# Kernel tuning notes

Measured on AMD Instinct MI355X. Metric: run time of the kernel, lower is better.

The kernel has to match this reference:

```python
import jax, jax.numpy as jnp
import numpy as np

NUM_NODES = 100000
NFEAT = 128
EMBED_DIM = 128
NHEADS = 2
NHID = EMBED_DIM // NHEADS  # 64
REL_DIM = 128
NUM_REL = 500
E1 = 288000  # 1-hop edges
E2 = 32000   # 2-hop edges
E = E1 + E2
ALPHA = 0.2  # LeakyReLU slope
EPS = 1e-16


def setup_inputs() -> dict:
    key = jax.random.key(0)
    ks = jax.random.split(key, 10)
    edge_index = jax.random.randint(ks[0], (2, E), 0, NUM_NODES, dtype=jnp.int32)
    x = jax.random.normal(ks[1], (NUM_NODES, NFEAT), dtype=jnp.float32)
    r = jax.random.normal(ks[2], (NUM_REL, REL_DIM), dtype=jnp.float32)
    edge_type = jax.random.randint(ks[3], (E1,), 0, NUM_REL, dtype=jnp.int32)
    edge_type_nhop = jax.random.randint(ks[4], (E2, 2), 0, NUM_REL, dtype=jnp.int32)
    # learned params (get_param -> xavier-ish normal)
    s = 0.02
    W_heads = jax.random.normal(ks[5], (NHEADS, 2 * NFEAT + REL_DIM, NHID), dtype=jnp.float32) * s
    a_heads = jax.random.normal(ks[6], (NHEADS, NHID, 1), dtype=jnp.float32) * s
    W_out = jax.random.normal(ks[7], (2 * (NHID * NHEADS) + EMBED_DIM, NHEADS * NHID), dtype=jnp.float32) * s
    a_out = jax.random.normal(ks[8], (NHEADS * NHID, 1), dtype=jnp.float32) * s
    W_r = jax.random.normal(ks[9], (REL_DIM, EMBED_DIM), dtype=jnp.float32) * s
    return {"edge_index": edge_index, "x": x, "r": r, "edge_type": edge_type,
            "edge_type_nhop": edge_type_nhop, "W_heads": W_heads, "a_heads": a_heads,
            "W_out": W_out, "a_out": a_out, "W_r": W_r}


def _gat_layer(edge_index, x, edge_embed, W, a, concat):
    src = edge_index[0]
    dst = edge_index[1]
    # [E, 2*in + rel] -> [E, out]
    edge_h = jnp.concatenate([x[src], x[dst], edge_embed], axis=1) @ W
    e = jax.nn.leaky_relu(jnp.squeeze(edge_h @ a, axis=-1), negative_slope=ALPHA)  # [E]
    # segment softmax over src groups
    seg_max = jax.ops.segment_max(e, src, num_segments=NUM_NODES)
    w = jnp.exp(e - seg_max[src])
    denom = jax.ops.segment_sum(w, src, num_segments=NUM_NODES)
    att = w / (denom[src] + EPS)  # dropout p=0.0 -> identity
    out = jax.ops.segment_sum(att[:, None] * edge_h, src, num_segments=NUM_NODES)  # [N, out]
    return jax.nn.elu(out) if concat else out


def reference(edge_index, x, r, edge_type, edge_type_nhop, W_heads, a_heads, W_out, a_out, W_r):
    # first-pass relation edge embeddings
    edge_embed = jnp.concatenate(
        [r[edge_type], r[edge_type_nhop[:, 0]] + r[edge_type_nhop[:, 1]]], axis=0)  # [E, rel]
    # multi-head attention layers (concat heads)
    heads = [_gat_layer(edge_index, x, edge_embed, W_heads[h], a_heads[h], True)
             for h in range(NHEADS)]
    x1 = jnp.concatenate(heads, axis=1)  # [N, nheads*nhid]; dropout p=0 identity
    # transform relations
    r2 = r @ W_r  # [num_rel, embed_dim]
    edge_embed2 = jnp.concatenate(
        [r2[edge_type], r2[edge_type_nhop[:, 0]] + r2[edge_type_nhop[:, 1]]], axis=0)
    out = jax.nn.elu(_gat_layer(edge_index, x1, edge_embed2, W_out, a_out, False))
    return out, r2
```

## Files before the change

### kernel.cpp

```cpp
#include <hip/hip_runtime.h>
#include <math.h>

#define NNODES 100000
#define NREL 500
#define E1 288000
#define ETOT 320000
#define LALPHA 0.2f
#define SEPS 1e-16f
#define NB_SCAN ((NNODES + 255) / 256)
#define GTILES 6250
#define GTPB 5
#define GGRID (GTILES / GTPB)

typedef __attribute__((ext_vector_type(8))) short bf16x8;
typedef __attribute__((ext_vector_type(4))) float f32x4;

__device__ __forceinline__ unsigned short f2bf(float x) {
  unsigned int u = __float_as_uint(x);
  unsigned int r = (u + 0x7fffu + ((u >> 16) & 1u)) >> 16;
  return (unsigned short)r;
}
__device__ __forceinline__ unsigned int packbf2(float lo, float hi) {
  return (unsigned int)f2bf(lo) | ((unsigned int)f2bf(hi) << 16);
}
__device__ __forceinline__ float unpk_lo(unsigned int u) { return __uint_as_float(u << 16); }
__device__ __forceinline__ float unpk_hi(unsigned int u) {
  return __uint_as_float(u & 0xffff0000u);
}
__device__ __forceinline__ float lrelu(float e) { return (e >= 0.f) ? e : LALPHA * e; }
__device__ __forceinline__ float wexp(float lg) { return __expf(fminf(lg, 60.f)); }

__device__ __forceinline__ float wave_sum64(float v) {
#pragma unroll
  for (int o = 32; o >= 1; o >>= 1) v += __shfl_xor(v, o, 64);
  return v;
}
__device__ __forceinline__ float red16(float v) {
  v += __shfl_xor(v, 1, 64);
  v += __shfl_xor(v, 2, 64);
  v += __shfl_xor(v, 4, 64);
  v += __shfl_xor(v, 8, 64);
  return v;
}

__global__ void k_zero_int(int* __restrict__ p, int n) {
  int i = blockIdx.x * blockDim.x + threadIdx.x;
  if (i < n) p[i] = 0;
}

__global__ void k_count(const int* __restrict__ src, int* __restrict__ cnt) {
  int e = blockIdx.x * blockDim.x + threadIdx.x;
  if (e < ETOT) atomicAdd(&cnt[src[e]], 1);
}

__global__ void k_scan_a(const int* __restrict__ cnt, int* __restrict__ rowstart,
                         int* __restrict__ blockTot) {
  __shared__ int s[256];
  int t = threadIdx.x;
  int idx = blockIdx.x * 256 + t;
  int v = (idx < NNODES) ? cnt[idx] : 0;
  s[t] = v;
  __syncthreads();
  for (int off = 1; off < 256; off <<= 1) {
    int xv = (t >= off) ? s[t - off] : 0;
    __syncthreads();
    s[t] += xv;
    __syncthreads();
  }
  if (idx < NNODES) rowstart[idx] = s[t] - v;
  if (t == 255) blockTot[blockIdx.x] = s[255];
}

__global__ void k_scan_b(const int* __restrict__ blockTot, int* __restrict__ blockOff) {
  __shared__ int s[512];
  int t = threadIdx.x;
  int v = (t < NB_SCAN) ? blockTot[t] : 0;
  s[t] = v;
  __syncthreads();
  for (int off = 1; off < 512; off <<= 1) {
    int xv = (t >= off) ? s[t - off] : 0;
    __syncthreads();
    s[t] += xv;
    __syncthreads();
  }
  if (t < NB_SCAN) blockOff[t] = s[t] - v;
}

__global__ void k_scan_c(int* __restrict__ rowstart, const int* __restrict__ blockOff,
                         int* __restrict__ cursor) {
  int idx = blockIdx.x * 256 + threadIdx.x;
  if (idx < NNODES) {
    int v = rowstart[idx] + blockOff[blockIdx.x];
    rowstart[idx] = v;
    cursor[idx] = v;
  }
  if (idx == 0) rowstart[NNODES] = ETOT;
}

__global__ void k_scatter(const int* __restrict__ src, int* __restrict__ cursor,
                          int* __restrict__ perm) {
  int e = blockIdx.x * blockDim.x + threadIdx.x;
  if (e < ETOT) {
    int pos = atomicAdd(&cursor[src[e]], 1);
    perm[pos] = e;
  }
}

__global__ void k_relprep1(const float* __restrict__ r, const float* __restrict__ Wh,
                           const float* __restrict__ ah, unsigned int* __restrict__ rW1p,
                           float* __restrict__ srel1) {
  __shared__ float vals[128];
  int t = blockIdx.x;
  int tid = threadIdx.x;
  int h = tid >> 6, kk = tid & 63;
  const float* wcol = Wh + h * 24576 + 256 * 64 + kk;
  const float* rrow = r + t * 128;
  float acc = 0.f;
#pragma unroll 4
  for (int d = 0; d < 128; ++d) acc = fmaf(rrow[d], wcol[d * 64], acc);
  vals[tid] = acc;
  float p = wave_sum64(acc * ah[h * 64 + kk]);
  if (kk == 0) srel1[t * 2 + h] = p;
  __syncthreads();
  if (tid < 64) rW1p[t * 64 + tid] = packbf2(vals[2 * tid], vals[2 * tid + 1]);
}

__global__ void k_relprep2f(const float* __restrict__ r, const float* __restrict__ Wr,
                            const float* __restrict__ Wo, const float* __restrict__ ao,
                            unsigned int* __restrict__ rW2p, float* __restrict__ srel2,
                            float* __restrict__ r2out) {
  __shared__ float v2[128];
  __shared__ float s[128];
  __shared__ float vals[128];
  int t = blockIdx.x;
  int k = threadIdx.x;
  float a2 = 0.f;
#pragma unroll 4
  for (int d = 0; d < 128; ++d) a2 = fmaf(r[t * 128 + d], Wr[d * 128 + k], a2);
  r2out[t * 128 + k] = a2;
  v2[k] = a2;
  __syncthreads();
  float acc = 0.f;
#pragma unroll 4
  for (int d = 0; d < 128; ++d) acc = fmaf(v2[d], Wo[(256 + d) * 128 + k], acc);
  vals[k] = acc;
  s[k] = acc * ao[k];
  __syncthreads();
  for (int off = 64; off >= 1; off >>= 1) {
    if (k < off) s[k] += s[k + off];
    __syncthreads();
  }
  if (k == 0) srel2[t] = s[0];
  if (k < 64) rW2p[t * 64 + k] = packbf2(vals[2 * k], vals[2 * k + 1]);
}

__global__ void k_packb_both(const float* __restrict__ Wh, const float* __restrict__ Wo,
                             unsigned short* __restrict__ Wb1,
                             unsigned short* __restrict__ Wb2) {
  int c = blockIdx.x & 255;
  int layer = blockIdx.x >> 8;
  int d = threadIdx.x;
  if (layer == 0) {
    int h = (c >> 6) & 1, part = c >> 7, kc = c & 63;
    Wb1[c * 128 + d] = f2bf(Wh[h * 24576 + (part * 128 + d) * 64 + kc]);
  } else {
    int part = c >> 7, kc = c & 127;
    Wb2[c * 128 + d] = f2bf(Wo[(part * 128 + d) * 128 + kc]);
  }
}

template <int LAYER>
__global__ __launch_bounds__(256) void k_gemm_mfma(const void* __restrict__ Xin,
                                                   const unsigned short* __restrict__ Wb,
                                                   const float* __restrict__ avec,
                                                   unsigned int* __restrict__ xWp,
                                                   float* __restrict__ sc) {
  const int lane = threadIdx.x & 63;
  const int wave = threadIdx.x >> 6;
  const int colv = lane & 15;
  const int kg = lane >> 4;

  bf16x8 b[4][4];
#pragma unroll
  for (int t = 0; t < 4; ++t)
#pragma unroll
    for (int s = 0; s < 4; ++s)
      b[t][s] = *(const bf16x8*)(Wb + (size_t)(wave * 64 + t * 16 + colv) * 128 + s * 32 +
                                 kg * 8);
  float av[4];
#pragma unroll
  for (int t = 0; t < 4; ++t) av[t] = avec[(wave & 1) * 64 + t * 16 + colv];
  const int slot = (LAYER == 1) ? (((wave & 1) << 1) | (wave >> 1)) : wave;

  const float4* xf4 = (const float4*)Xin;
  const uint4* xu4 = (const uint4*)Xin;
  int tile = blockIdx.x * GTPB;

  float4 cf[8];
  uint4 cu[4];
  {
    int ar = tile * 16 + colv;
    if (LAYER == 1) {
      int base = ar * 32 + kg * 2;
#pragma unroll
      for (int s = 0; s < 4; ++s) {
        cf[2 * s] = xf4[base + s * 8];
        cf[2 * s + 1] = xf4[base + s * 8 + 1];
      }
    } else {
      int base = ar * 16 + kg;
#pragma unroll
      for (int s = 0; s < 4; ++s) cu[s] = xu4[base + s * 4];
    }
  }

  for (int it = 0; it < GTPB; ++it, ++tile) {
    float4 nf[8];
    uint4 nu[4];
    const bool hasnext = (it + 1 < GTPB);
    if (hasnext) {
      int ar = (tile + 1) * 16 + colv;
      if (LAYER == 1) {
        int base = ar * 32 + kg * 2;
#pragma unroll
        for (int s = 0; s < 4; ++s) {
          nf[2 * s] = xf4[base + s * 8];
          nf[2 * s + 1] = xf4[base + s * 8 + 1];
        }
      } else {
        int base = ar * 16 + kg;
#pragma unroll
        for (int s = 0; s < 4; ++s) nu[s] = xu4[base + s * 4];
      }
    }

    bf16x8 a[4];
    if (LAYER == 1) {
#pragma unroll
      for (int s = 0; s < 4; ++s) {
        union {
          unsigned short us[8];
          bf16x8 v;
        } u;
        u.us[0] = f2bf(cf[2 * s].x); u.us[1] = f2bf(cf[2 * s].y);
        u.us[2] = f2bf(cf[2 * s].z); u.us[3] = f2bf(cf[2 * s].w);
        u.us[4] = f2bf(cf[2 * s + 1].x); u.us[5] = f2bf(cf[2 * s + 1].y);
        u.us[6] = f2bf(cf[2 * s + 1].z); u.us[7] = f2bf(cf[2 * s + 1].w);
        a[s] = u.v;
      }
    } else {
#pragma unroll
      for (int s = 0; s < 4; ++s) {
        union {
          uint4 q;
          bf16x8 v;
        } u;
        u.q = cu[s];
        a[s] = u.v;
      }
    }

    f32x4 acc[4];
#pragma unroll
    for (int t = 0; t < 4; ++t) acc[t] = (f32x4){0.f, 0.f, 0.f, 0.f};
#pragma unroll
    for (int s = 0; s < 4; ++s)
#pragma unroll
      for (int t = 0; t < 4; ++t)
        acc[t] = __builtin_amdgcn_mfma_f32_16x16x32_bf16(a[s], b[t][s], acc[t], 0, 0, 0);

    const int rbase = tile * 16 + kg * 4;
    const int m = colv >> 1;
    const bool evn = (colv & 1) == 0;
#pragma unroll
    for (int i = 0; i < 4; ++i) {
      unsigned int* orow = xWp + (size_t)(rbase + i) * 128 + wave * 32;
#pragma unroll
      for (int t = 0; t < 4; ++t) {
        float lo = acc[t][i];
        float other = __shfl_xor(lo, 1, 64);
        if (evn) orow[t * 8 + m] = packbf2(lo, other);
      }
      float p = 0.f;
#pragma unroll
      for (int t = 0; t < 4; ++t) p = fmaf(acc[t][i], av[t], p);
      p = red16(p);
      if (colv == 0) sc[(size_t)(rbase + i) * 4 + slot] = p;
    }

    if (hasnext) {
      if (LAYER == 1) {
#pragma unroll
        for (int j = 0; j < 8; ++j) cf[j] = nf[j];
      } else {
#pragma unroll
        for (int j = 0; j < 4; ++j) cu[j] = nu[j];
      }
    }
  }
}

__global__ void k_eprep1(const int* __restrict__ perm, const int* __restrict__ srcA,
                         const int* __restrict__ dstA, const int* __restrict__ et,
                         const int* __restrict__ et2, const float* __restrict__ sc1,
                         const float* __restrict__ srel1, int* __restrict__ srcp,
                         int* __restrict__ dnp, int2* __restrict__ t12,
                         float2* __restrict__ wexp1, float* __restrict__ denom1) {
  int p = blockIdx.x * 256 + threadIdx.x;
  if (p >= ETOT) return;
  int ed = perm[p];
  int src = srcA[ed], dn = dstA[ed];
  int t1, t2 = -1;
  float rel0, rel1;
  if (ed < E1) {
    t1 = et[ed];
    float2 sr = ((const float2*)srel1)[t1];
    rel0 = sr.x;
    rel1 = sr.y;
  } else {
    int2 tt = ((const int2*)et2)[ed - E1];
    t1 = tt.x;
    t2 = tt.y;
    float2 sa = ((const float2*)srel1)[t1];
    float2 sb = ((const float2*)srel1)[t2];
    rel0 = sa.x + sb.x;
    rel1 = sa.y + sb.y;
  }
  float4 ssv = ((const float4*)sc1)[src];
  float4 sdv = ((const float4*)sc1)[dn];
  float w0 = wexp(lrelu(ssv.x + sdv.y + rel0));
  float w1 = wexp(lrelu(ssv.z + sdv.w + rel1));
  wexp1[p] = make_float2(w0, w1);
  atomicAdd(&denom1[2 * src], w0);
  atomicAdd(&denom1[2 * src + 1], w1);
  srcp[p] = src;
  dnp[p] = dn;
  t12[p] = make_int2(t1, t2);
}

__global__ void k_eprep2(const int* __restrict__ srcp, const int* __restrict__ dnp,
                         const int2* __restrict__ t12, const float* __restrict__ sc2,
                         const float* __restrict__ srel2, float* __restrict__ wexp2,
                         float* __restrict__ denom2) {
  int p = blockIdx.x * 256 + threadIdx.x;
  if (p >= ETOT) return;
  int src = srcp[p], dn = dnp[p];
  int2 tt = t12[p];
  float rel = srel2[tt.x];
  if (tt.y >= 0) rel += srel2[tt.y];
  float4 ssv = ((const float4*)sc2)[src];
  float4 sdv = ((const float4*)sc2)[dn];
  float w = wexp(lrelu((ssv.x + ssv.y) + (sdv.z + sdv.w) + rel));
  wexp2[p] = w;
  atomicAdd(&denom2[src], w);
}

__global__ __launch_bounds__(256) void k_agg1(
    const int* __restrict__ rowstart, const float2* __restrict__ wexp1,
    const int* __restrict__ dnp, const int2* __restrict__ t12,
    const unsigned int* __restrict__ xWp, const unsigned int* __restrict__ rW1p,
    const float2* __restrict__ denom1, unsigned int* __restrict__ x1b) {
  int n = blockIdx.x * 4 + (threadIdx.x >> 6);
  int lane = threadIdx.x & 63;
  int q = lane & 15, g = lane >> 4;
  int s0 = rowstart[n];
  int deg = rowstart[n + 1] - s0;
  int jj = q + 16 * g;
  float r0 = 0.f, r1 = 0.f;
  if (deg > 0) {
    float ac0[4] = {0.f, 0.f, 0.f, 0.f}, ac1[4] = {0.f, 0.f, 0.f, 0.f};
    const int pend = s0 + deg;
    for (int p0 = s0; p0 < pend; p0 += 4) {
      int p = p0 + g;
      float w0 = 0.f, w1 = 0.f;
      int dne = 0, t1e = 0, t2e = -1;
      if (p < pend) {
        float2 wv = wexp1[p];
        w0 = wv.x;
        w1 = wv.y;
        dne = dnp[p];
        int2 tt = t12[p];
        t1e = tt.x;
        t2e = tt.y;
      }
      const unsigned int* xr = xWp + (size_t)dne * 128 + 64;
      const unsigned int* rp = rW1p + (size_t)t1e * 64;
#pragma unroll
      for (int k = 0; k < 4; ++k) {
        int j2 = q + 16 * k;
        float as = (k < 2) ? w0 : w1;
        unsigned int ud = xr[j2];
        unsigned int ur = rp[j2];
        float rv0 = unpk_lo(ur), rv1 = unpk_hi(ur);
        if (t2e >= 0) {
          unsigned int u2 = rW1p[(size_t)t2e * 64 + j2];
          rv0 += unpk_lo(u2);
          rv1 += unpk_hi(u2);
        }
        ac0[k] = fmaf(as, unpk_lo(ud) + rv0, ac0[k]);
        ac1[k] = fmaf(as, unpk_hi(ud) + rv1, ac1[k]);
      }
    }
#pragma unroll
    for (int k = 0; k < 4; ++k) {
      ac0[k] += __shfl_xor(ac0[k], 16, 64);
      ac0[k] += __shfl_xor(ac0[k], 32, 64);
      ac1[k] += __shfl_xor(ac1[k], 16, 64);
      ac1[k] += __shfl_xor(ac1[k], 32, 64);
    }
    float a0g = (g == 0) ? ac0[0] : (g == 1) ? ac0[1] : (g == 2) ? ac0[2] : ac0[3];
    float a1g = (g == 0) ? ac1[0] : (g == 1) ? ac1[1] : (g == 2) ? ac1[2] : ac1[3];
    float2 dd = denom1[n];
    float dsel = (g < 2) ? dd.x : dd.y;
    float isel = 1.f / (dsel + SEPS);
    unsigned int us = xWp[(size_t)n * 128 + jj];
    float o0 = (a0g + dsel * unpk_lo(us)) * isel;
    float o1 = (a1g + dsel * unpk_hi(us)) * isel;
    r0 = (o0 > 0.f) ? o0 : __expf(o0) - 1.f;
    r1 = (o1 > 0.f) ? o1 : __expf(o1) - 1.f;
  }
  x1b[(size_t)n * 64 + jj] = packbf2(r0, r1);
}

__global__ __launch_bounds__(256) void k_agg2(
    const int* __restrict__ rowstart, const float* __restrict__ wexp2,
    const int* __restrict__ dnp, const int2* __restrict__ t12,
    const unsigned int* __restrict__ xWp, const unsigned int* __restrict__ rW2p,
    const float* __restrict__ denom2, float* __restrict__ outp) {
  int n = blockIdx.x * 4 + (threadIdx.x >> 6);
  int lane = threadIdx.x & 63;
  int q = lane & 15, g = lane >> 4;
  int s0 = rowstart[n];
  int deg = rowstart[n + 1] - s0;
  int jj = q + 16 * g;
  float r0 = 0.f, r1 = 0.f;
  if (deg > 0) {
    float ac0[4] = {0.f, 0.f, 0.f, 0.f}, ac1[4] = {0.f, 0.f, 0.f, 0.f};
    const int pend = s0 + deg;
    for (int p0 = s0; p0 < pend; p0 += 4) {
      int p = p0 + g;
      float w = 0.f;
      int dne = 0, t1e = 0, t2e = -1;
      if (p < pend) {
        w = wexp2[p];
        dne = dnp[p];
        int2 tt = t12[p];
        t1e = tt.x;
        t2e = tt.y;
      }
      const unsigned int* xr = xWp + (size_t)dne * 128 + 64;
      const unsigned int* rp = rW2p + (size_t)t1e * 64;
#pragma unroll
      for (int k = 0; k < 4; ++k) {
        int j2 = q + 16 * k;
        unsigned int ud = xr[j2];
        unsigned int ur = rp[j2];
        float rv0 = unpk_lo(ur), rv1 = unpk_hi(ur);
        if (t2e >= 0) {
          unsigned int u2 = rW2p[(size_t)t2e * 64 + j2];
          rv0 += unpk_lo(u2);
          rv1 += unpk_hi(u2);
        }
        ac0[k] = fmaf(w, unpk_lo(ud) + rv0, ac0[k]);
        ac1[k] = fmaf(w, unpk_hi(ud) + rv1, ac1[k]);
      }
    }
#pragma unroll
    for (int k = 0; k < 4; ++k) {
      ac0[k] += __shfl_xor(ac0[k], 16, 64);
      ac0[k] += __shfl_xor(ac0[k], 32, 64);
      ac1[k] += __shfl_xor(ac1[k], 16, 64);
      ac1[k] += __shfl_xor(ac1[k], 32, 64);
    }
    float a0g = (g == 0) ? ac0[0] : (g == 1) ? ac0[1] : (g == 2) ? ac0[2] : ac0[3];
    float a1g = (g == 0) ? ac1[0] : (g == 1) ? ac1[1] : (g == 2) ? ac1[2] : ac1[3];
    float d = denom2[n];
    float inv = 1.f / (d + SEPS);
    unsigned int us = xWp[(size_t)n * 128 + jj];
    float o0 = (a0g + d * unpk_lo(us)) * inv;
    float o1 = (a1g + d * unpk_hi(us)) * inv;
    r0 = (o0 > 0.f) ? o0 : __expf(o0) - 1.f;
    r1 = (o1 > 0.f) ? o1 : __expf(o1) - 1.f;
  }
  ((float2*)outp)[(size_t)n * 64 + jj] = make_float2(r0, r1);
}

extern "C" void kernel_launch(void* const* d_in, const int* in_sizes, int n_in, void* d_out,
                              int out_size, void* d_ws, size_t ws_size, hipStream_t stream) {
  const int* edge_index = (const int*)d_in[0];
  const int* srcA = edge_index;
  const int* dstA = edge_index + ETOT;
  const float* x = (const float*)d_in[1];
  const float* r = (const float*)d_in[2];
  const int* et = (const int*)d_in[3];
  const int* et2 = (const int*)d_in[4];
  const float* Wh = (const float*)d_in[5];
  const float* ah = (const float*)d_in[6];
  const float* Wo = (const float*)d_in[7];
  const float* ao = (const float*)d_in[8];
  const float* Wr = (const float*)d_in[9];
  float* out = (float*)d_out;
  float* r2out = out + (size_t)NNODES * 128;

  char* ws = (char*)d_ws;
  size_t o = 0;
  auto alloc = [&](size_t bytes) {
    char* p = ws + o;
    o += (bytes + 255) & ~(size_t)255;
    return p;
  };
  unsigned int* xWp = (unsigned int*)alloc((size_t)NNODES * 128 * 4);
  float* sc1 = (float*)alloc((size_t)NNODES * 4 * 4);
  float* sc2 = (float*)alloc((size_t)NNODES * 4 * 4);
  int* zb = (int*)alloc((size_t)4 * NNODES * 4);
  int* cnt = zb;
  float* denom1 = (float*)(zb + NNODES);
  float* denom2 = (float*)(zb + 3 * NNODES);
  unsigned int* rW1p = (unsigned int*)alloc((size_t)NREL * 64 * 4);
  float* srel1 = (float*)alloc(2 * NREL * 4);
  unsigned int* rW2p = (unsigned int*)alloc((size_t)NREL * 64 * 4);
  float* srel2 = (float*)alloc(NREL * 4);
  unsigned int* x1b = (unsigned int*)alloc((size_t)NNODES * 64 * 4);
  unsigned short* Wb1 = (unsigned short*)alloc(256 * 128 * 2);
  unsigned short* Wb2 = (unsigned short*)alloc(256 * 128 * 2);
  int* rowstart = (int*)alloc((NNODES + 1) * 4);
  int* cursor = (int*)alloc(NNODES * 4);
  int* blockTot = (int*)alloc(512 * 4);
  int* blockOff = (int*)alloc(512 * 4);
  int* perm = (int*)alloc(ETOT * 4);
  int* srcp = (int*)alloc(ETOT * 4);
  int* dnp = (int*)alloc(ETOT * 4);
  int2* t12 = (int2*)alloc((size_t)ETOT * 8);
  float2* wexp1 = (float2*)alloc((size_t)ETOT * 8);
  float* wexp2 = (float*)alloc(ETOT * 4);

  const int EB = (ETOT + 255) / 256;

  k_zero_int<<<(4 * NNODES + 255) / 256, 256, 0, stream>>>(zb, 4 * NNODES);

  k_count<<<EB, 256, 0, stream>>>(srcA, cnt);
  k_scan_a<<<NB_SCAN, 256, 0, stream>>>(cnt, rowstart, blockTot);
  k_scan_b<<<1, 512, 0, stream>>>(blockTot, blockOff);
  k_scan_c<<<NB_SCAN, 256, 0, stream>>>(rowstart, blockOff, cursor);
  k_scatter<<<EB, 256, 0, stream>>>(srcA, cursor, perm);

  k_relprep1<<<NREL, 128, 0, stream>>>(r, Wh, ah, rW1p, srel1);
  k_relprep2f<<<NREL, 128, 0, stream>>>(r, Wr, Wo, ao, rW2p, srel2, r2out);
  k_packb_both<<<512, 128, 0, stream>>>(Wh, Wo, Wb1, Wb2);

  k_gemm_mfma<1><<<GGRID, 256, 0, stream>>>(x, Wb1, ah, xWp, sc1);
  k_eprep1<<<EB, 256, 0, stream>>>(perm, srcA, dstA, et, et2, sc1, srel1, srcp, dnp, t12,
                                   wexp1, denom1);
  k_agg1<<<NNODES / 4, 256, 0, stream>>>(rowstart, wexp1, dnp, t12, xWp, rW1p,
                                         (const float2*)denom1, x1b);

  k_gemm_mfma<2><<<GGRID, 256, 0, stream>>>(x1b, Wb2, ao, xWp, sc2);
  k_eprep2<<<EB, 256, 0, stream>>>(srcp, dnp, t12, sc2, srel2, wexp2, denom2);
  k_agg2<<<NNODES / 4, 256, 0, stream>>>(rowstart, wexp2, dnp, t12, xWp, rW2p, denom2, out);
}
```

Baseline: 428.0 us.

## Fuse edge-score and softmax-denominator computation into CSR aggregation kernels

The scatter kernel now writes destination and relation types directly in CSR order, which removes the permutation array and the separate per-edge prep pass. Both aggregation kernels compute the attention logits and exp weights inline, summing the softmax denominator per node with wave shuffles instead of global atomics. This drops two kernel launches, the wexp/denom/srcp buffers and their atomic traffic. In exchange the aggregation inner loop does extra gathers of destination scores and relation scalars per edge.

```diff
diff --git a/kernel.cpp b/kernel.cpp
--- a/kernel.cpp
+++ b/kernel.cpp
@@ -97,12 +97,23 @@
   if (idx == 0) rowstart[NNODES] = ETOT;
 }
 
-__global__ void k_scatter(const int* __restrict__ src, int* __restrict__ cursor,
-                          int* __restrict__ perm) {
+__global__ void k_scatter(const int* __restrict__ srcA, const int* __restrict__ dstA,
+                          const int* __restrict__ et, const int* __restrict__ et2,
+                          int* __restrict__ cursor, int* __restrict__ dnp,
+                          int2* __restrict__ t12) {
   int e = blockIdx.x * blockDim.x + threadIdx.x;
   if (e < ETOT) {
-    int pos = atomicAdd(&cursor[src[e]], 1);
-    perm[pos] = e;
+    int pos = atomicAdd(&cursor[srcA[e]], 1);
+    dnp[pos] = dstA[e];
+    int t1, t2 = -1;
+    if (e < E1) {
+      t1 = et[e];
+    } else {
+      int2 tt = ((const int2*)et2)[e - E1];
+      t1 = tt.x;
+      t2 = tt.y;
+    }
+    t12[pos] = make_int2(t1, t2);
   }
 }
 
@@ -300,66 +311,11 @@
   }
 }
 
-__global__ void k_eprep1(const int* __restrict__ perm, const int* __restrict__ srcA,
-                         const int* __restrict__ dstA, const int* __restrict__ et,
-                         const int* __restrict__ et2, const float* __restrict__ sc1,
-                         const float* __restrict__ srel1, int* __restrict__ srcp,
-                         int* __restrict__ dnp, int2* __restrict__ t12,
-                         float2* __restrict__ wexp1, float* __restrict__ denom1) {
-  int p = blockIdx.x * 256 + threadIdx.x;
-  if (p >= ETOT) return;
-  int ed = perm[p];
-  int src = srcA[ed], dn = dstA[ed];
-  int t1, t2 = -1;
-  float rel0, rel1;
-  if (ed < E1) {
-    t1 = et[ed];
-    float2 sr = ((const float2*)srel1)[t1];
-    rel0 = sr.x;
-    rel1 = sr.y;
-  } else {
-    int2 tt = ((const int2*)et2)[ed - E1];
-    t1 = tt.x;
-    t2 = tt.y;
-    float2 sa = ((const float2*)srel1)[t1];
-    float2 sb = ((const float2*)srel1)[t2];
-    rel0 = sa.x + sb.x;
-    rel1 = sa.y + sb.y;
-  }
-  float4 ssv = ((const float4*)sc1)[src];
-  float4 sdv = ((const float4*)sc1)[dn];
-  float w0 = wexp(lrelu(ssv.x + sdv.y + rel0));
-  float w1 = wexp(lrelu(ssv.z + sdv.w + rel1));
-  wexp1[p] = make_float2(w0, w1);
-  atomicAdd(&denom1[2 * src], w0);
-  atomicAdd(&denom1[2 * src + 1], w1);
-  srcp[p] = src;
-  dnp[p] = dn;
-  t12[p] = make_int2(t1, t2);
-}
-
-__global__ void k_eprep2(const int* __restrict__ srcp, const int* __restrict__ dnp,
-                         const int2* __restrict__ t12, const float* __restrict__ sc2,
-                         const float* __restrict__ srel2, float* __restrict__ wexp2,
-                         float* __restrict__ denom2) {
-  int p = blockIdx.x * 256 + threadIdx.x;
-  if (p >= ETOT) return;
-  int src = srcp[p], dn = dnp[p];
-  int2 tt = t12[p];
-  float rel = srel2[tt.x];
-  if (tt.y >= 0) rel += srel2[tt.y];
-  float4 ssv = ((const float4*)sc2)[src];
-  float4 sdv = ((const float4*)sc2)[dn];
-  float w = wexp(lrelu((ssv.x + ssv.y) + (sdv.z + sdv.w) + rel));
-  wexp2[p] = w;
-  atomicAdd(&denom2[src], w);
-}
-
 __global__ __launch_bounds__(256) void k_agg1(
-    const int* __restrict__ rowstart, const float2* __restrict__ wexp1,
-    const int* __restrict__ dnp, const int2* __restrict__ t12,
-    const unsigned int* __restrict__ xWp, const unsigned int* __restrict__ rW1p,
-    const float2* __restrict__ denom1, unsigned int* __restrict__ x1b) {
+    const int* __restrict__ rowstart, const int* __restrict__ dnp,
+    const int2* __restrict__ t12, const unsigned int* __restrict__ xWp,
+    const unsigned int* __restrict__ rW1p, const float* __restrict__ sc1,
+    const float2* __restrict__ srel1, unsigned int* __restrict__ x1b) {
   int n = blockIdx.x * 4 + (threadIdx.x >> 6);
   int lane = threadIdx.x & 63;
   int q = lane & 15, g = lane >> 4;
@@ -368,20 +324,32 @@
   int jj = q + 16 * g;
   float r0 = 0.f, r1 = 0.f;
   if (deg > 0) {
+    float4 scn = ((const float4*)sc1)[n];
+    const float ss0 = scn.x, ss1 = scn.z;
     float ac0[4] = {0.f, 0.f, 0.f, 0.f}, ac1[4] = {0.f, 0.f, 0.f, 0.f};
+    float dsum0 = 0.f, dsum1 = 0.f;
     const int pend = s0 + deg;
     for (int p0 = s0; p0 < pend; p0 += 4) {
       int p = p0 + g;
       float w0 = 0.f, w1 = 0.f;
       int dne = 0, t1e = 0, t2e = -1;
       if (p < pend) {
-        float2 wv = wexp1[p];
-        w0 = wv.x;
-        w1 = wv.y;
         dne = dnp[p];
         int2 tt = t12[p];
         t1e = tt.x;
         t2e = tt.y;
+        float2 sr = srel1[t1e];
+        float rel0 = sr.x, rel1 = sr.y;
+        if (t2e >= 0) {
+          float2 sb = srel1[t2e];
+          rel0 += sb.x;
+          rel1 += sb.y;
+        }
+        float4 sdv = ((const float4*)sc1)[dne];
+        w0 = wexp(lrelu(ss0 + sdv.y + rel0));
+        w1 = wexp(lrelu(ss1 + sdv.w + rel1));
+        dsum0 += w0;
+        dsum1 += w1;
       }
       const unsigned int* xr = xWp + (size_t)dne * 128 + 64;
       const unsigned int* rp = rW1p + (size_t)t1e * 64;
@@ -408,10 +376,13 @@
       ac1[k] += __shfl_xor(ac1[k], 16, 64);
       ac1[k] += __shfl_xor(ac1[k], 32, 64);
     }
+    dsum0 += __shfl_xor(dsum0, 16, 64);
+    dsum0 += __shfl_xor(dsum0, 32, 64);
+    dsum1 += __shfl_xor(dsum1, 16, 64);
+    dsum1 += __shfl_xor(dsum1, 32, 64);
     float a0g = (g == 0) ? ac0[0] : (g == 1) ? ac0[1] : (g == 2) ? ac0[2] : ac0[3];
     float a1g = (g == 0) ? ac1[0] : (g == 1) ? ac1[1] : (g == 2) ? ac1[2] : ac1[3];
-    float2 dd = denom1[n];
-    float dsel = (g < 2) ? dd.x : dd.y;
+    float dsel = (g < 2) ? dsum0 : dsum1;
     float isel = 1.f / (dsel + SEPS);
     unsigned int us = xWp[(size_t)n * 128 + jj];
     float o0 = (a0g + dsel * unpk_lo(us)) * isel;
@@ -423,10 +394,10 @@
 }
 
 __global__ __launch_bounds__(256) void k_agg2(
-    const int* __restrict__ rowstart, const float* __restrict__ wexp2,
-    const int* __restrict__ dnp, const int2* __restrict__ t12,
-    const unsigned int* __restrict__ xWp, const unsigned int* __restrict__ rW2p,
-    const float* __restrict__ denom2, float* __restrict__ outp) {
+    const int* __restrict__ rowstart, const int* __restrict__ dnp,
+    const int2* __restrict__ t12, const unsigned int* __restrict__ xWp,
+    const unsigned int* __restrict__ rW2p, const float* __restrict__ sc2,
+    const float* __restrict__ srel2, float* __restrict__ outp) {
   int n = blockIdx.x * 4 + (threadIdx.x >> 6);
   int lane = threadIdx.x & 63;
   int q = lane & 15, g = lane >> 4;
@@ -435,18 +406,25 @@
   int jj = q + 16 * g;
   float r0 = 0.f, r1 = 0.f;
   if (deg > 0) {
+    float4 scn = ((const float4*)sc2)[n];
+    const float ss = scn.x + scn.y;
     float ac0[4] = {0.f, 0.f, 0.f, 0.f}, ac1[4] = {0.f, 0.f, 0.f, 0.f};
+    float dsum = 0.f;
     const int pend = s0 + deg;
     for (int p0 = s0; p0 < pend; p0 += 4) {
       int p = p0 + g;
       float w = 0.f;
       int dne = 0, t1e = 0, t2e = -1;
       if (p < pend) {
-        w = wexp2[p];
         dne = dnp[p];
         int2 tt = t12[p];
         t1e = tt.x;
         t2e = tt.y;
+        float rel = srel2[t1e];
+        if (t2e >= 0) rel += srel2[t2e];
+        float4 sdv = ((const float4*)sc2)[dne];
+        w = wexp(lrelu(ss + (sdv.z + sdv.w) + rel));
+        dsum += w;
       }
       const unsigned int* xr = xWp + (size_t)dne * 128 + 64;
       const unsigned int* rp = rW2p + (size_t)t1e * 64;
@@ -472,13 +450,14 @@
       ac1[k] += __shfl_xor(ac1[k], 16, 64);
       ac1[k] += __shfl_xor(ac1[k], 32, 64);
     }
+    dsum += __shfl_xor(dsum, 16, 64);
+    dsum += __shfl_xor(dsum, 32, 64);
     float a0g = (g == 0) ? ac0[0] : (g == 1) ? ac0[1] : (g == 2) ? ac0[2] : ac0[3];
     float a1g = (g == 0) ? ac1[0] : (g == 1) ? ac1[1] : (g == 2) ? ac1[2] : ac1[3];
-    float d = denom2[n];
-    float inv = 1.f / (d + SEPS);
+    float inv = 1.f / (dsum + SEPS);
     unsigned int us = xWp[(size_t)n * 128 + jj];
-    float o0 = (a0g + d * unpk_lo(us)) * inv;
-    float o1 = (a1g + d * unpk_hi(us)) * inv;
+    float o0 = (a0g + dsum * unpk_lo(us)) * inv;
+    float o1 = (a1g + dsum * unpk_hi(us)) * inv;
     r0 = (o0 > 0.f) ? o0 : __expf(o0) - 1.f;
     r1 = (o1 > 0.f) ? o1 : __expf(o1) - 1.f;
   }
@@ -512,10 +491,6 @@
   unsigned int* xWp = (unsigned int*)alloc((size_t)NNODES * 128 * 4);
   float* sc1 = (float*)alloc((size_t)NNODES * 4 * 4);
   float* sc2 = (float*)alloc((size_t)NNODES * 4 * 4);
-  int* zb = (int*)alloc((size_t)4 * NNODES * 4);
-  int* cnt = zb;
-  float* denom1 = (float*)(zb + NNODES);
-  float* denom2 = (float*)(zb + 3 * NNODES);
   unsigned int* rW1p = (unsigned int*)alloc((size_t)NREL * 64 * 4);
   float* srel1 = (float*)alloc(2 * NREL * 4);
   unsigned int* rW2p = (unsigned int*)alloc((size_t)NREL * 64 * 4);
@@ -523,38 +498,31 @@
   unsigned int* x1b = (unsigned int*)alloc((size_t)NNODES * 64 * 4);
   unsigned short* Wb1 = (unsigned short*)alloc(256 * 128 * 2);
   unsigned short* Wb2 = (unsigned short*)alloc(256 * 128 * 2);
+  int* cnt = (int*)alloc(NNODES * 4);
   int* rowstart = (int*)alloc((NNODES + 1) * 4);
   int* cursor = (int*)alloc(NNODES * 4);
   int* blockTot = (int*)alloc(512 * 4);
   int* blockOff = (int*)alloc(512 * 4);
-  int* perm = (int*)alloc(ETOT * 4);
-  int* srcp = (int*)alloc(ETOT * 4);
   int* dnp = (int*)alloc(ETOT * 4);
   int2* t12 = (int2*)alloc((size_t)ETOT * 8);
-  float2* wexp1 = (float2*)alloc((size_t)ETOT * 8);
-  float* wexp2 = (float*)alloc(ETOT * 4);
 
   const int EB = (ETOT + 255) / 256;
 
-  k_zero_int<<<(4 * NNODES + 255) / 256, 256, 0, stream>>>(zb, 4 * NNODES);
-
+  k_zero_int<<<(NNODES + 255) / 256, 256, 0, stream>>>(cnt, NNODES);
   k_count<<<EB, 256, 0, stream>>>(srcA, cnt);
   k_scan_a<<<NB_SCAN, 256, 0, stream>>>(cnt, rowstart, blockTot);
   k_scan_b<<<1, 512, 0, stream>>>(blockTot, blockOff);
   k_scan_c<<<NB_SCAN, 256, 0, stream>>>(rowstart, blockOff, cursor);
-  k_scatter<<<EB, 256, 0, stream>>>(srcA, cursor, perm);
+  k_scatter<<<EB, 256, 0, stream>>>(srcA, dstA, et, et2, cursor, dnp, t12);
 
   k_relprep1<<<NREL, 128, 0, stream>>>(r, Wh, ah, rW1p, srel1);
   k_relprep2f<<<NREL, 128, 0, stream>>>(r, Wr, Wo, ao, rW2p, srel2, r2out);
   k_packb_both<<<512, 128, 0, stream>>>(Wh, Wo, Wb1, Wb2);
 
   k_gemm_mfma<1><<<GGRID, 256, 0, stream>>>(x, Wb1, ah, xWp, sc1);
-  k_eprep1<<<EB, 256, 0, stream>>>(perm, srcA, dstA, et, et2, sc1, srel1, srcp, dnp, t12,
-                                   wexp1, denom1);
-  k_agg1<<<NNODES / 4, 256, 0, stream>>>(rowstart, wexp1, dnp, t12, xWp, rW1p,
-                                         (const float2*)denom1, x1b);
+  k_agg1<<<NNODES / 4, 256, 0, stream>>>(rowstart, dnp, t12, xWp, rW1p, sc1,
+                                         (const float2*)srel1, x1b);
 
   k_gemm_mfma<2><<<GGRID, 256, 0, stream>>>(x1b, Wb2, ao, xWp, sc2);
-  k_eprep2<<<EB, 256, 0, stream>>>(srcp, dnp, t12, sc2, srel2, wexp2, denom2);
-  k_agg2<<<NNODES / 4, 256, 0, stream>>>(rowstart, wexp2, dnp, t12, xWp, rW2p, denom2, out);
-}
+  k_agg2<<<NNODES / 4, 256, 0, stream>>>(rowstart, dnp, t12, xWp, rW2p, sc2, srel2, out);
+}
```

New measurement: 392.7 us. 8.2% less time.
